# Performance work log

Measured on AMD Instinct MI355X. Metric: run time of the kernel, lower is better.

## Reference

```python
import jax, jax.numpy as jnp
import numpy as np

B, S, H, E, I_E, V = 4, 4096, 1024, 8, 512, 100000


def setup_inputs() -> dict:
    key = jax.random.key(0)
    k0, k1, k2, k3, k4, k5, k6 = jax.random.split(key, 7)
    hidden_states = jax.random.normal(k0, (B, S, H), dtype=jnp.float32)
    token_ids = jax.random.randint(k1, (B, S), 0, V, dtype=jnp.int64)
    mu = jax.random.normal(k2, (B, S, H), dtype=jnp.float32)
    # torch Linear(in,out,bias=False) weight is [out,in]; we store transposed [in,out]
    w_gate = jax.random.normal(k3, (E, H, I_E), dtype=jnp.float32) * 0.02
    w_up = jax.random.normal(k4, (E, H, I_E), dtype=jnp.float32) * 0.02
    w_down = jax.random.normal(k5, (E, I_E, H), dtype=jnp.float32) * 0.02
    # module zero-inits mu_router; use small random so the mu-override path is exercised
    mu_router_w = jax.random.normal(k6, (E, H), dtype=jnp.float32) * 0.02
    return {
        "hidden_states": hidden_states,
        "token_ids": token_ids,
        "mu": mu,
        "w_gate": w_gate,
        "w_up": w_up,
        "w_down": w_down,
        "mu_router_w": mu_router_w,
    }


def reference(hidden_states, token_ids, mu, w_gate, w_up, w_down, mu_router_w):
    num_experts = w_gate.shape[0]
    # deterministic token->expert mapping: token_id % num_experts (after clamp)
    tid = jnp.clip(token_ids, 0, V - 1)
    base_expert_ids = (tid % num_experts).astype(jnp.int32)  # [B,S]
    # mu-guided override: one_hot*10 + mu_logits, argmax
    mu_logits = jnp.einsum("bsh,eh->bse", mu, mu_router_w)
    base_one_hot = jax.nn.one_hot(base_expert_ids, num_experts, dtype=mu_logits.dtype)
    expert_ids = jnp.argmax(base_one_hot * 10.0 + mu_logits, axis=-1)  # [B,S]

    x = hidden_states.reshape(-1, H)          # [T,H], T=B*S
    eid = expert_ids.reshape(-1)              # [T]
    out = jnp.zeros_like(x)
    for e in range(num_experts):
        mask = (eid == e)[:, None]            # [T,1]
        g = x @ w_gate[e]                     # [T,I_E]
        u = x @ w_up[e]                       # [T,I_E]
        y = (jax.nn.silu(g) * u) @ w_down[e]  # [T,H] SwiGLU
        out = out + jnp.where(mask, y, 0.0)
    return out.reshape(hidden_states.shape)
```

## Files before the change

kernel.cpp:

```cpp
#include <hip/hip_runtime.h>
#include <stdint.h>

#define T_TOK   16384
#define H_DIM   1024
#define IE_DIM  512
#define E_NUM   8
#define V_MAX   100000

typedef __attribute__((ext_vector_type(8))) short bf16x8;
typedef __attribute__((ext_vector_type(4))) float f32x4;
typedef unsigned long long ull;

__device__ __forceinline__ unsigned short f2bf(float f) {
  union { float f; unsigned u; } v; v.f = f;
  unsigned r = v.u + 0x7fffu + ((v.u >> 16) & 1u);
  return (unsigned short)(r >> 16);
}

__device__ __forceinline__ void gload16(const void* g, void* l) {
  __builtin_amdgcn_global_load_lds(
      (const __attribute__((address_space(1))) unsigned int*)g,
      (__attribute__((address_space(3))) unsigned int*)(unsigned int)(uintptr_t)l,
      16, 0, 0);
}

__global__ __launch_bounds__(256) void k_pre(
    const float* __restrict__ mu, const int* __restrict__ tok,
    const float* __restrict__ mrw, int* __restrict__ eid,
    int* __restrict__ blockCnt,
    const float* __restrict__ wg, const float* __restrict__ wu,
    const float* __restrict__ wd, unsigned short* __restrict__ WgT,
    unsigned short* __restrict__ WuT, unsigned short* __restrict__ WdT) {
  __shared__ unsigned short lds[64][72];
  int tid = threadIdx.x;

  if (blockIdx.x < 1024) {
    int* cnt = (int*)&lds[0][0];
    if (tid < 8) cnt[tid] = 0;
    int wv = blockIdx.x * 4 + (tid >> 6);
    int t0 = wv * 4;
    int lane = tid & 63;
    const float4* mrw4 = (const float4*)mrw;

    float acc[4][E_NUM];
#pragma unroll
    for (int i = 0; i < 4; i++)
#pragma unroll
      for (int e = 0; e < E_NUM; e++) acc[i][e] = 0.f;

#pragma unroll
    for (int j = 0; j < 4; j++) {
      int idx = lane + 64 * j;
      float4 wr[E_NUM];
#pragma unroll
      for (int e = 0; e < E_NUM; e++) wr[e] = mrw4[e * 256 + idx];
#pragma unroll
      for (int i = 0; i < 4; i++) {
        float4 m = ((const float4*)(mu + (size_t)(t0 + i) * H_DIM))[idx];
#pragma unroll
        for (int e = 0; e < E_NUM; e++)
          acc[i][e] += m.x * wr[e].x + m.y * wr[e].y + m.z * wr[e].z + m.w * wr[e].w;
      }
    }
#pragma unroll
    for (int i = 0; i < 4; i++)
#pragma unroll
      for (int e = 0; e < E_NUM; e++)
#pragma unroll
        for (int off = 32; off >= 1; off >>= 1)
          acc[i][e] += __shfl_xor(acc[i][e], off, 64);

    __syncthreads();
#pragma unroll
    for (int i = 0; i < 4; i++) {
      int tv = tok[t0 + i];
      if (tv < 0) tv = 0;
      if (tv > V_MAX - 1) tv = V_MAX - 1;
      int base = tv & 7;
      int best = 0; float bs = -1e30f;
#pragma unroll
      for (int e = 0; e < E_NUM; e++) {
        float s = acc[i][e] + (e == base ? 10.f : 0.f);
        if (s > bs) { bs = s; best = e; }
      }
      if (lane == i) {
        eid[t0 + i] = best;
        atomicAdd(&cnt[best], 1);
      }
    }
    __syncthreads();
    if (tid < 8) blockCnt[blockIdx.x * 8 + tid] = cnt[tid];
  } else {
    int sel = (blockIdx.x - 1024) >> 10;
    int blk = blockIdx.x & 1023;
    const float* src; unsigned short* dst; int R, C;
    if (sel == 0)      { src = wg; dst = WgT; R = H_DIM; C = IE_DIM; }
    else if (sel == 1) { src = wu; dst = WuT; R = H_DIM; C = IE_DIM; }
    else               { src = wd; dst = WdT; R = IE_DIM; C = H_DIM; }
    int tpe = (R >> 6) * (C >> 6);
    int e = blk / tpe;
    int rem = blk % tpe;
    int tr = rem / (C >> 6);
    int tc = rem % (C >> 6);
    const float* s = src + (size_t)e * R * C;
    unsigned short* d = dst + (size_t)e * R * C;
    int r0 = tid >> 4;
    int c0 = (tid & 15) * 4;
#pragma unroll
    for (int i = 0; i < 4; i++) {
      int r = r0 + i * 16;
      float4 v = *(const float4*)(s + (size_t)(tr * 64 + r) * C + tc * 64 + c0);
      lds[r][c0 + 0] = f2bf(v.x); lds[r][c0 + 1] = f2bf(v.y);
      lds[r][c0 + 2] = f2bf(v.z); lds[r][c0 + 3] = f2bf(v.w);
    }
    __syncthreads();
    int oc = tid >> 2;
    int ob = (tid & 3) * 16;
    unsigned short tmp[16];
#pragma unroll
    for (int i = 0; i < 16; i++) tmp[i] = lds[ob + i][oc];
    uint4* dp = (uint4*)(d + (size_t)(tc * 64 + oc) * R + tr * 64 + ob);
    dp[0] = ((uint4*)tmp)[0];
    dp[1] = ((uint4*)tmp)[1];
  }
}

__global__ __launch_bounds__(1024) void k_scan2(
    const int* __restrict__ blockCnt, int* __restrict__ blockBase,
    int* __restrict__ offsets, int* __restrict__ tileOff,
    int* __restrict__ tileOff128) {
  int b = threadIdx.x;
  __shared__ ull s0[1024], s1[1024];
  __shared__ int offL[8];
  const int4* p = (const int4*)(blockCnt + b * 8);
  int4 x0 = p[0], x1 = p[1];
  int c[8] = {x0.x, x0.y, x0.z, x0.w, x1.x, x1.y, x1.z, x1.w};
  ull v0 = (ull)c[0] | ((ull)c[1] << 16) | ((ull)c[2] << 32) | ((ull)c[3] << 48);
  ull v1 = (ull)c[4] | ((ull)c[5] << 16) | ((ull)c[6] << 32) | ((ull)c[7] << 48);
  s0[b] = v0; s1[b] = v1;
  __syncthreads();
  for (int st = 1; st < 1024; st <<= 1) {
    ull a0 = 0, a1 = 0;
    if (b >= st) { a0 = s0[b - st]; a1 = s1[b - st]; }
    __syncthreads();
    v0 += a0; v1 += a1;
    s0[b] = v0; s1[b] = v1;
    __syncthreads();
  }
  if (b == 1023) {
    int tot[8];
#pragma unroll
    for (int e = 0; e < 4; e++) tot[e] = (int)((v0 >> (16 * e)) & 0xFFFF);
#pragma unroll
    for (int e = 0; e < 4; e++) tot[4 + e] = (int)((v1 >> (16 * e)) & 0xFFFF);
    int s = 0, ts = 0, ts2 = 0;
    for (int e = 0; e < E_NUM; e++) {
      offsets[e] = s; offL[e] = s;
      tileOff[e] = ts; tileOff128[e] = ts2;
      s += tot[e];
      ts += (tot[e] + 255) >> 8;
      ts2 += (tot[e] + 127) >> 7;
    }
    offsets[E_NUM] = s; tileOff[E_NUM] = ts; tileOff128[E_NUM] = ts2;
  }
  __syncthreads();
  int be[8];
#pragma unroll
  for (int e = 0; e < 4; e++)
    be[e] = offL[e] + (int)((v0 >> (16 * e)) & 0xFFFF) - c[e];
#pragma unroll
  for (int e = 0; e < 4; e++)
    be[4 + e] = offL[4 + e] + (int)((v1 >> (16 * e)) & 0xFFFF) - c[4 + e];
  int4* q = (int4*)(blockBase + b * 8);
  q[0] = make_int4(be[0], be[1], be[2], be[3]);
  q[1] = make_int4(be[4], be[5], be[6], be[7]);
}

__global__ __launch_bounds__(256) void k_gather(
    const float* __restrict__ hs, const int* __restrict__ eid,
    const int* __restrict__ blockBase, int* __restrict__ tokofrow,
    unsigned short* __restrict__ Xs) {
  int b = blockIdx.x;
  int tid = threadIdx.x;
  __shared__ int eL[16];
  __shared__ int posL[16];
  if (tid < 16) eL[tid] = eid[b * 16 + tid];
  __syncthreads();
  if (tid < 16) {
    int e = eL[tid];
    int r = 0;
    for (int j = 0; j < tid; j++) r += (eL[j] == e);
    int pos = blockBase[b * 8 + e] + r;
    posL[tid] = pos;
    tokofrow[pos] = b * 16 + tid;
  }
  __syncthreads();
  int w = tid >> 6, lane = tid & 63;
#pragma unroll
  for (int i = 0; i < 4; i++) {
    int li = w * 4 + i;
    int t = b * 16 + li;
    int pos = posL[li];
    const float4* src = (const float4*)(hs + (size_t)t * H_DIM);
    unsigned short* drow = Xs + (size_t)pos * H_DIM;
#pragma unroll
    for (int j = 0; j < 4; j++) {
      float4 v = src[lane + 64 * j];
      ushort4 bb;
      bb.x = f2bf(v.x); bb.y = f2bf(v.y); bb.z = f2bf(v.z); bb.w = f2bf(v.w);
      *(ushort4*)(drow + (lane + 64 * j) * 4) = bb;
    }
  }
}

__global__ __launch_bounds__(512, 1) void k_gemm1(
    const unsigned short* __restrict__ Xs,
    const unsigned short* __restrict__ WgT,
    const unsigned short* __restrict__ WuT,
    unsigned short* __restrict__ Hb,
    const int* __restrict__ offsets, const int* __restrict__ tileOff) {
  int bid0 = blockIdx.x;
  int xcd = bid0 & 7, seq = bid0 >> 3;
  int wg = (xcd < 4 ? xcd * 36 : 144 + (xcd - 4) * 35) + seq;
  int nt = wg & 3;
  int mlin = wg >> 2;
  if (mlin >= tileOff[E_NUM]) return;
  int e = 0;
#pragma unroll
  for (int i = 1; i < E_NUM; i++)
    if (mlin >= tileOff[i]) e = i;
  int mtile = mlin - tileOff[e];
  int segStart = offsets[e], segEnd = offsets[e + 1];
  int M = segEnd - segStart;

  __shared__ unsigned short Alds[2][256 * 64];
  __shared__ unsigned short Bglds[2][128 * 64];
  __shared__ unsigned short Bulds[2][128 * 64];

  int tid = threadIdx.x;
  int lane = tid & 63;
  int w = tid >> 6;
  int wm = w >> 1;
  int wn = w & 1;
  int r0 = lane & 15;
  int kcb = lane >> 4;

  f32x4 accg[4][4], accu[4][4];
#pragma unroll
  for (int i = 0; i < 4; i++)
#pragma unroll
    for (int j = 0; j < 4; j++) {
      accg[i][j] = (f32x4)(0.f);
      accu[i][j] = (f32x4)(0.f);
    }

  const unsigned short* Asrc[4];
#pragma unroll
  for (int i = 0; i < 4; i++) {
    int s = tid + i * 512;
    int row = s >> 3;
    int ch = (s & 7) ^ (row & 7);
    int gr = mtile * 256 + row; if (gr > M - 1) gr = M - 1;
    Asrc[i] = Xs + (size_t)(segStart + gr) * H_DIM + ch * 8;
  }
  const unsigned short* Bgsrc[2];
  const unsigned short* Busrc[2];
#pragma unroll
  for (int i = 0; i < 2; i++) {
    int s = tid + i * 512;
    int row = s >> 3;
    int ch = (s & 7) ^ (row & 7);
    Bgsrc[i] = WgT + (size_t)e * IE_DIM * H_DIM + (size_t)(nt * 128 + row) * H_DIM + ch * 8;
    Busrc[i] = WuT + (size_t)e * IE_DIM * H_DIM + (size_t)(nt * 128 + row) * H_DIM + ch * 8;
  }

#define GLA(i, kt, buf) gload16(Asrc[i] + (kt) * 64, (char*)Alds[buf] + (tid + (i) * 512) * 16)
#define GLG(i, kt, buf) gload16(Bgsrc[i] + (kt) * 64, (char*)Bglds[buf] + (tid + (i) * 512) * 16)
#define GLU(i, kt, buf) gload16(Busrc[i] + (kt) * 64, (char*)Bulds[buf] + (tid + (i) * 512) * 16)

  int aoff[4][2], boff[4][2];
#pragma unroll
  for (int mf = 0; mf < 4; mf++) {
    int row = wm * 64 + mf * 16 + r0;
#pragma unroll
    for (int ks = 0; ks < 2; ks++) {
      int c = ks * 4 + kcb;
      aoff[mf][ks] = row * 128 + ((c ^ (row & 7)) << 4);
    }
  }
#pragma unroll
  for (int nf = 0; nf < 4; nf++) {
    int row = wn * 64 + nf * 16 + r0;
#pragma unroll
    for (int ks = 0; ks < 2; ks++) {
      int c = ks * 4 + kcb;
      boff[nf][ks] = row * 128 + ((c ^ (row & 7)) << 4);
    }
  }

  const int NT = H_DIM / 64;
  GLA(0, 0, 0); GLA(1, 0, 0); GLA(2, 0, 0); GLA(3, 0, 0);
  GLG(0, 0, 0); GLG(1, 0, 0); GLU(0, 0, 0); GLU(1, 0, 0);

  bf16x8 a0[2][2], a1[2][2], bb[4][2];

  for (int kt = 0; kt < NT; kt++) {
    int buf = kt & 1, nbuf = buf ^ 1;
    int ktn = (kt + 1 < NT) ? kt + 1 : 0;
    const char* Ab = (const char*)Alds[buf];
    const char* Bgb = (const char*)Bglds[buf];
    const char* Bub = (const char*)Bulds[buf];

    __builtin_amdgcn_s_barrier();
    GLA(0, ktn, nbuf); GLA(1, ktn, nbuf); GLA(2, ktn, nbuf); GLA(3, ktn, nbuf);
    GLG(0, ktn, nbuf); GLG(1, ktn, nbuf); GLU(0, ktn, nbuf); GLU(1, ktn, nbuf);
    asm volatile("s_waitcnt vmcnt(8)" ::: "memory");
    __builtin_amdgcn_s_barrier();

#pragma unroll
    for (int mf = 0; mf < 2; mf++)
#pragma unroll
      for (int ks = 0; ks < 2; ks++)
        a0[mf][ks] = *(const bf16x8*)(Ab + aoff[mf][ks]);
#pragma unroll
    for (int nf = 0; nf < 4; nf++)
#pragma unroll
      for (int ks = 0; ks < 2; ks++)
        bb[nf][ks] = *(const bf16x8*)(Bgb + boff[nf][ks]);
    asm volatile("s_waitcnt lgkmcnt(0)" ::: "memory");
    __builtin_amdgcn_sched_barrier(0);
    __builtin_amdgcn_s_setprio(1);
#pragma unroll
    for (int mf = 0; mf < 2; mf++)
#pragma unroll
      for (int nf = 0; nf < 4; nf++)
#pragma unroll
        for (int ks = 0; ks < 2; ks++)
          accg[mf][nf] = __builtin_amdgcn_mfma_f32_16x16x32_bf16(
              a0[mf][ks], bb[nf][ks], accg[mf][nf], 0, 0, 0);
    __builtin_amdgcn_s_setprio(0);

#pragma unroll
    for (int mf = 0; mf < 2; mf++)
#pragma unroll
      for (int ks = 0; ks < 2; ks++)
        a1[mf][ks] = *(const bf16x8*)(Ab + aoff[2 + mf][ks]);
    asm volatile("s_waitcnt lgkmcnt(0)" ::: "memory");
    __builtin_amdgcn_sched_barrier(0);
    __builtin_amdgcn_s_setprio(1);
#pragma unroll
    for (int mf = 0; mf < 2; mf++)
#pragma unroll
      for (int nf = 0; nf < 4; nf++)
#pragma unroll
        for (int ks = 0; ks < 2; ks++)
          accg[2 + mf][nf] = __builtin_amdgcn_mfma_f32_16x16x32_bf16(
              a1[mf][ks], bb[nf][ks], accg[2 + mf][nf], 0, 0, 0);
    __builtin_amdgcn_s_setprio(0);

#pragma unroll
    for (int nf = 0; nf < 4; nf++)
#pragma unroll
      for (int ks = 0; ks < 2; ks++)
        bb[nf][ks] = *(const bf16x8*)(Bub + boff[nf][ks]);
    asm volatile("s_waitcnt lgkmcnt(0)" ::: "memory");
    __builtin_amdgcn_sched_barrier(0);
    __builtin_amdgcn_s_setprio(1);
#pragma unroll
    for (int mf = 0; mf < 2; mf++)
#pragma unroll
      for (int nf = 0; nf < 4; nf++)
#pragma unroll
        for (int ks = 0; ks < 2; ks++)
          accu[mf][nf] = __builtin_amdgcn_mfma_f32_16x16x32_bf16(
              a0[mf][ks], bb[nf][ks], accu[mf][nf], 0, 0, 0);
    __builtin_amdgcn_s_setprio(0);

    __builtin_amdgcn_s_setprio(1);
#pragma unroll
    for (int mf = 0; mf < 2; mf++)
#pragma unroll
      for (int nf = 0; nf < 4; nf++)
#pragma unroll
        for (int ks = 0; ks < 2; ks++)
          accu[2 + mf][nf] = __builtin_amdgcn_mfma_f32_16x16x32_bf16(
              a1[mf][ks], bb[nf][ks], accu[2 + mf][nf], 0, 0, 0);
    __builtin_amdgcn_s_setprio(0);
  }
  asm volatile("s_waitcnt vmcnt(0)" ::: "memory");
#undef GLA
#undef GLG
#undef GLU

  int rowBase = segStart + mtile * 256 + wm * 64;
#pragma unroll
  for (int mf = 0; mf < 4; mf++)
#pragma unroll
    for (int nf = 0; nf < 4; nf++) {
      int col = nt * 128 + wn * 64 + nf * 16 + r0;
#pragma unroll
      for (int j = 0; j < 4; j++) {
        int r = rowBase + mf * 16 + (lane >> 4) * 4 + j;
        if (r < segEnd) {
          float g = accg[mf][nf][j];
          float u = accu[mf][nf][j];
          float h = (g / (1.f + __expf(-g))) * u;
          Hb[(size_t)r * IE_DIM + col] = f2bf(h);
        }
      }
    }
}

__global__ __launch_bounds__(512) void k_gemm2(
    const unsigned short* __restrict__ Hb,
    const unsigned short* __restrict__ WdT,
    float* __restrict__ out,
    const int* __restrict__ offsets, const int* __restrict__ tileOff,
    const int* __restrict__ tokofrow) {
  int bid0 = blockIdx.x;
  int wg = (bid0 & 7) * 135 + (bid0 >> 3);
  int nt = wg & 7;
  int mlin = wg >> 3;
  if (mlin >= tileOff[E_NUM]) return;
  int e = 0;
#pragma unroll
  for (int i = 1; i < E_NUM; i++)
    if (mlin >= tileOff[i]) e = i;
  int mtile = mlin - tileOff[e];
  int segStart = offsets[e], segEnd = offsets[e + 1];
  int M = segEnd - segStart;

  __shared__ unsigned short Alds[3][128 * 32];
  __shared__ unsigned short Blds[3][128 * 32];

  int tid = threadIdx.x;
  int lane = tid & 63;
  int w = tid >> 6;
  int wm = w >> 2;
  int wn = w & 3;

  f32x4 acc[4][2];
#pragma unroll
  for (int i = 0; i < 4; i++)
#pragma unroll
    for (int j = 0; j < 2; j++) acc[i][j] = (f32x4)(0.f);

  int sr = tid >> 2;
  int sc = tid & 3;
  int scc = sc ^ ((sr >> 1) & 3);
  int grow = mtile * 128 + sr;
  if (grow > M - 1) grow = M - 1;
  const unsigned short* Arow = Hb + (size_t)(segStart + grow) * IE_DIM + scc * 8;
  const unsigned short* Brow =
      WdT + (size_t)e * H_DIM * IE_DIM + (size_t)(nt * 128 + sr) * IE_DIM + scc * 8;

#define STAGE2(buf, k0)                                            \
  {                                                                \
    gload16(Arow + (k0), (char*)Alds[buf] + tid * 16);             \
    gload16(Brow + (k0), (char*)Blds[buf] + tid * 16);             \
  }

  int kc = lane >> 4;
  int arow[4], browv[2];
#pragma unroll
  for (int mf = 0; mf < 4; mf++) arow[mf] = wm * 64 + mf * 16 + (lane & 15);
#pragma unroll
  for (int nf = 0; nf < 2; nf++) browv[nf] = wn * 32 + nf * 16 + (lane & 15);

  const int NT = IE_DIM / 32;
  STAGE2(0, 0);
  STAGE2(1, 32);

  int cur = 0;
  for (int t = 0; t < NT; t++) {
    asm volatile("s_waitcnt vmcnt(2)" ::: "memory");
    __builtin_amdgcn_s_barrier();
    __builtin_amdgcn_sched_barrier(0);
    int tn = t + 2; if (tn >= NT) tn -= NT;
    int nbuf = cur + 2; if (nbuf >= 3) nbuf -= 3;
    STAGE2(nbuf, tn * 32);

    bf16x8 a[4], b[2];
#pragma unroll
    for (int mf = 0; mf < 4; mf++) {
      int row = arow[mf];
      int byte = row * 64 + ((kc ^ ((row >> 1) & 3)) << 4);
      a[mf] = *(const bf16x8*)((const char*)Alds[cur] + byte);
    }
#pragma unroll
    for (int nf = 0; nf < 2; nf++) {
      int row = browv[nf];
      int byte = row * 64 + ((kc ^ ((row >> 1) & 3)) << 4);
      b[nf] = *(const bf16x8*)((const char*)Blds[cur] + byte);
    }
    __builtin_amdgcn_s_setprio(1);
#pragma unroll
    for (int mf = 0; mf < 4; mf++)
#pragma unroll
      for (int nf = 0; nf < 2; nf++)
        acc[mf][nf] = __builtin_amdgcn_mfma_f32_16x16x32_bf16(
            a[mf], b[nf], acc[mf][nf], 0, 0, 0);
    __builtin_amdgcn_s_setprio(0);
    cur = (cur + 1 == 3) ? 0 : cur + 1;
  }
#undef STAGE2
  asm volatile("s_waitcnt vmcnt(0)" ::: "memory");

  int rowBase = segStart + mtile * 128 + wm * 64;
#pragma unroll
  for (int mf = 0; mf < 4; mf++)
#pragma unroll
    for (int nf = 0; nf < 2; nf++) {
      int col = nt * 128 + wn * 32 + nf * 16 + (lane & 15);
#pragma unroll
      for (int j = 0; j < 4; j++) {
        int r = rowBase + mf * 16 + (lane >> 4) * 4 + j;
        if (r < segEnd) {
          int t = tokofrow[r];
          out[(size_t)t * H_DIM + col] = acc[mf][nf][j];
        }
      }
    }
}

#define WS_XS    ((size_t)0)
#define WS_WGT   ((size_t)33554432)
#define WS_WUT   ((size_t)41943040)
#define WS_WDT   ((size_t)50331648)
#define WS_HB    ((size_t)58720256)
#define WS_EID   ((size_t)75497472)
#define WS_TOK   ((size_t)75563008)
#define WS_OFF   ((size_t)75628544)
#define WS_BC    ((size_t)75629568)
#define WS_BB    ((size_t)75662336)

extern "C" void kernel_launch(void* const* d_in, const int* in_sizes, int n_in,
                              void* d_out, int out_size, void* d_ws, size_t ws_size,
                              hipStream_t stream) {
  const float* hs  = (const float*)d_in[0];
  const int*   tok = (const int*)d_in[1];
  const float* mu  = (const float*)d_in[2];
  const float* wg  = (const float*)d_in[3];
  const float* wu  = (const float*)d_in[4];
  const float* wd  = (const float*)d_in[5];
  const float* mrw = (const float*)d_in[6];
  float* out = (float*)d_out;
  char* ws = (char*)d_ws;

  unsigned short* Xs  = (unsigned short*)(ws + WS_XS);
  unsigned short* WgT = (unsigned short*)(ws + WS_WGT);
  unsigned short* WuT = (unsigned short*)(ws + WS_WUT);
  unsigned short* WdT = (unsigned short*)(ws + WS_WDT);
  unsigned short* Hb  = (unsigned short*)(ws + WS_HB);
  int* eid      = (int*)(ws + WS_EID);
  int* tokofrow = (int*)(ws + WS_TOK);
  int* offsets   = (int*)(ws + WS_OFF);
  int* tileOff   = offsets + 16;
  int* tileOff128= offsets + 32;
  int* blockCnt = (int*)(ws + WS_BC);
  int* blockBase= (int*)(ws + WS_BB);

  k_pre<<<4096, 256, 0, stream>>>(mu, tok, mrw, eid, blockCnt,
                                  wg, wu, wd, WgT, WuT, WdT);
  k_scan2<<<1, 1024, 0, stream>>>(blockCnt, blockBase, offsets, tileOff, tileOff128);
  k_gather<<<1024, 256, 0, stream>>>(hs, eid, blockBase, tokofrow, Xs);
  k_gemm1<<<284, 512, 0, stream>>>(Xs, WgT, WuT, Hb, offsets, tileOff);
  k_gemm2<<<135 * 8, 512, 0, stream>>>(Hb, WdT, out, offsets, tileOff128, tokofrow);
}
```

Before: 169.0 us.

## Deepen gate/up GEMM pipeline to 4-stage K=32 buffers with interleaved loads

Rewrites the gate/up grouped GEMM main loop. It moves from a double-buffered K=64 tile to a quad-buffered K=32 ring, with prefetch three stages ahead. Global-to-LDS loads are split into four pieces (A halves, gate, up) and placed between MFMA phases, with a new 4-way XOR swizzle. The goal is deeper latency hiding and finer overlap of memory and compute. In exchange the loop has many more s_barriers per K step and the MFMA work per phase is smaller.

```diff
diff --git a/kernel.cpp b/kernel.cpp
--- a/kernel.cpp
+++ b/kernel.cpp
@@ -233,9 +233,9 @@
   int segStart = offsets[e], segEnd = offsets[e + 1];
   int M = segEnd - segStart;
 
-  __shared__ unsigned short Alds[2][256 * 64];
-  __shared__ unsigned short Bglds[2][128 * 64];
-  __shared__ unsigned short Bulds[2][128 * 64];
+  __shared__ unsigned short Alds[4][256 * 32];
+  __shared__ unsigned short Bglds[4][128 * 32];
+  __shared__ unsigned short Bulds[4][128 * 32];
 
   int tid = threadIdx.x;
   int lane = tid & 63;
@@ -254,143 +254,123 @@
       accu[i][j] = (f32x4)(0.f);
     }
 
-  const unsigned short* Asrc[4];
-#pragma unroll
-  for (int i = 0; i < 4; i++) {
-    int s = tid + i * 512;
-    int row = s >> 3;
-    int ch = (s & 7) ^ (row & 7);
-    int gr = mtile * 256 + row; if (gr > M - 1) gr = M - 1;
-    Asrc[i] = Xs + (size_t)(segStart + gr) * H_DIM + ch * 8;
-  }
-  const unsigned short* Bgsrc[2];
-  const unsigned short* Busrc[2];
-#pragma unroll
-  for (int i = 0; i < 2; i++) {
-    int s = tid + i * 512;
-    int row = s >> 3;
-    int ch = (s & 7) ^ (row & 7);
-    Bgsrc[i] = WgT + (size_t)e * IE_DIM * H_DIM + (size_t)(nt * 128 + row) * H_DIM + ch * 8;
-    Busrc[i] = WuT + (size_t)e * IE_DIM * H_DIM + (size_t)(nt * 128 + row) * H_DIM + ch * 8;
-  }
-
-#define GLA(i, kt, buf) gload16(Asrc[i] + (kt) * 64, (char*)Alds[buf] + (tid + (i) * 512) * 16)
-#define GLG(i, kt, buf) gload16(Bgsrc[i] + (kt) * 64, (char*)Bglds[buf] + (tid + (i) * 512) * 16)
-#define GLU(i, kt, buf) gload16(Busrc[i] + (kt) * 64, (char*)Bulds[buf] + (tid + (i) * 512) * 16)
-
-  int aoff[4][2], boff[4][2];
+  int arow0 = tid >> 2;
+  int arow1 = arow0 + 128;
+  int acs = (tid & 3) ^ ((arow0 >> 1) & 3);
+  int ga0 = mtile * 256 + arow0; if (ga0 > M - 1) ga0 = M - 1;
+  int ga1 = mtile * 256 + arow1; if (ga1 > M - 1) ga1 = M - 1;
+  const unsigned short* Aad0 = Xs + (size_t)(segStart + ga0) * H_DIM + acs * 8;
+  const unsigned short* Aad1 = Xs + (size_t)(segStart + ga1) * H_DIM + acs * 8;
+  int brow = tid >> 2;
+  int bcs = (tid & 3) ^ ((brow >> 1) & 3);
+  const unsigned short* Bgad =
+      WgT + (size_t)e * IE_DIM * H_DIM + (size_t)(nt * 128 + brow) * H_DIM + bcs * 8;
+  const unsigned short* Buad =
+      WuT + (size_t)e * IE_DIM * H_DIM + (size_t)(nt * 128 + brow) * H_DIM + bcs * 8;
+
+#define SGA0(h) gload16(Aad0 + ((h) & 31) * 32, (char*)Alds + ((h) & 3) * 16384 + tid * 16)
+#define SGA1(h) gload16(Aad1 + ((h) & 31) * 32, (char*)Alds + ((h) & 3) * 16384 + 8192 + tid * 16)
+#define SGG(h)  gload16(Bgad + ((h) & 31) * 32, (char*)Bglds + ((h) & 3) * 8192 + tid * 16)
+#define SGU(h)  gload16(Buad + ((h) & 31) * 32, (char*)Bulds + ((h) & 3) * 8192 + tid * 16)
+
+  int aoff[4], boff[4];
 #pragma unroll
   for (int mf = 0; mf < 4; mf++) {
     int row = wm * 64 + mf * 16 + r0;
-#pragma unroll
-    for (int ks = 0; ks < 2; ks++) {
-      int c = ks * 4 + kcb;
-      aoff[mf][ks] = row * 128 + ((c ^ (row & 7)) << 4);
-    }
+    aoff[mf] = row * 64 + ((kcb ^ ((row >> 1) & 3)) << 4);
   }
 #pragma unroll
   for (int nf = 0; nf < 4; nf++) {
     int row = wn * 64 + nf * 16 + r0;
-#pragma unroll
-    for (int ks = 0; ks < 2; ks++) {
-      int c = ks * 4 + kcb;
-      boff[nf][ks] = row * 128 + ((c ^ (row & 7)) << 4);
-    }
-  }
-
-  const int NT = H_DIM / 64;
-  GLA(0, 0, 0); GLA(1, 0, 0); GLA(2, 0, 0); GLA(3, 0, 0);
-  GLG(0, 0, 0); GLG(1, 0, 0); GLU(0, 0, 0); GLU(1, 0, 0);
-
-  bf16x8 a0[2][2], a1[2][2], bb[4][2];
-
-  for (int kt = 0; kt < NT; kt++) {
-    int buf = kt & 1, nbuf = buf ^ 1;
-    int ktn = (kt + 1 < NT) ? kt + 1 : 0;
-    const char* Ab = (const char*)Alds[buf];
-    const char* Bgb = (const char*)Bglds[buf];
-    const char* Bub = (const char*)Bulds[buf];
-
-    __builtin_amdgcn_s_barrier();
-    GLA(0, ktn, nbuf); GLA(1, ktn, nbuf); GLA(2, ktn, nbuf); GLA(3, ktn, nbuf);
-    GLG(0, ktn, nbuf); GLG(1, ktn, nbuf); GLU(0, ktn, nbuf); GLU(1, ktn, nbuf);
-    asm volatile("s_waitcnt vmcnt(8)" ::: "memory");
-    __builtin_amdgcn_s_barrier();
-
-#pragma unroll
-    for (int mf = 0; mf < 2; mf++)
-#pragma unroll
-      for (int ks = 0; ks < 2; ks++)
-        a0[mf][ks] = *(const bf16x8*)(Ab + aoff[mf][ks]);
-#pragma unroll
-    for (int nf = 0; nf < 4; nf++)
-#pragma unroll
-      for (int ks = 0; ks < 2; ks++)
-        bb[nf][ks] = *(const bf16x8*)(Bgb + boff[nf][ks]);
-    asm volatile("s_waitcnt lgkmcnt(0)" ::: "memory");
-    __builtin_amdgcn_sched_barrier(0);
-    __builtin_amdgcn_s_setprio(1);
-#pragma unroll
-    for (int mf = 0; mf < 2; mf++)
-#pragma unroll
-      for (int nf = 0; nf < 4; nf++)
-#pragma unroll
-        for (int ks = 0; ks < 2; ks++)
+    boff[nf] = row * 64 + ((kcb ^ ((row >> 1) & 3)) << 4);
+  }
+
+  SGA0(0); SGA1(0); SGG(0); SGU(0);
+  SGA0(1); SGA1(1); SGG(1); SGU(1);
+  SGA0(2); SGA1(2); SGG(2); SGU(2);
+  asm volatile("s_waitcnt vmcnt(8)" ::: "memory");
+  __builtin_amdgcn_s_barrier();
+
+  const int NH = H_DIM / 32;
+  for (int hh = 0; hh < NH; hh += 4) {
+#pragma unroll
+    for (int u = 0; u < 4; u++) {
+      int h = hh + u;
+      const char* Ab  = (const char*)Alds + u * 16384;
+      const char* Bgb = (const char*)Bglds + u * 8192;
+      const char* Bub = (const char*)Bulds + u * 8192;
+      int hn = h + 3;
+      bf16x8 a[4], bg[4], bu[4];
+
+      a[0] = *(const bf16x8*)(Ab + aoff[0]);
+      a[1] = *(const bf16x8*)(Ab + aoff[1]);
+#pragma unroll
+      for (int nf = 0; nf < 4; nf++) bg[nf] = *(const bf16x8*)(Bgb + boff[nf]);
+      SGA0(hn);
+      __builtin_amdgcn_s_barrier();
+      asm volatile("s_waitcnt lgkmcnt(0)" ::: "memory");
+      __builtin_amdgcn_sched_barrier(0);
+      __builtin_amdgcn_s_setprio(1);
+#pragma unroll
+      for (int mf = 0; mf < 2; mf++)
+#pragma unroll
+        for (int nf = 0; nf < 4; nf++)
           accg[mf][nf] = __builtin_amdgcn_mfma_f32_16x16x32_bf16(
-              a0[mf][ks], bb[nf][ks], accg[mf][nf], 0, 0, 0);
-    __builtin_amdgcn_s_setprio(0);
-
-#pragma unroll
-    for (int mf = 0; mf < 2; mf++)
-#pragma unroll
-      for (int ks = 0; ks < 2; ks++)
-        a1[mf][ks] = *(const bf16x8*)(Ab + aoff[2 + mf][ks]);
-    asm volatile("s_waitcnt lgkmcnt(0)" ::: "memory");
-    __builtin_amdgcn_sched_barrier(0);
-    __builtin_amdgcn_s_setprio(1);
-#pragma unroll
-    for (int mf = 0; mf < 2; mf++)
-#pragma unroll
-      for (int nf = 0; nf < 4; nf++)
-#pragma unroll
-        for (int ks = 0; ks < 2; ks++)
+              a[mf], bg[nf], accg[mf][nf], 0, 0, 0);
+      __builtin_amdgcn_s_setprio(0);
+      __builtin_amdgcn_s_barrier();
+
+      a[2] = *(const bf16x8*)(Ab + aoff[2]);
+      a[3] = *(const bf16x8*)(Ab + aoff[3]);
+      SGA1(hn);
+      __builtin_amdgcn_s_barrier();
+      asm volatile("s_waitcnt lgkmcnt(0)" ::: "memory");
+      __builtin_amdgcn_sched_barrier(0);
+      __builtin_amdgcn_s_setprio(1);
+#pragma unroll
+      for (int mf = 0; mf < 2; mf++)
+#pragma unroll
+        for (int nf = 0; nf < 4; nf++)
           accg[2 + mf][nf] = __builtin_amdgcn_mfma_f32_16x16x32_bf16(
-              a1[mf][ks], bb[nf][ks], accg[2 + mf][nf], 0, 0, 0);
-    __builtin_amdgcn_s_setprio(0);
-
-#pragma unroll
-    for (int nf = 0; nf < 4; nf++)
-#pragma unroll
-      for (int ks = 0; ks < 2; ks++)
-        bb[nf][ks] = *(const bf16x8*)(Bub + boff[nf][ks]);
-    asm volatile("s_waitcnt lgkmcnt(0)" ::: "memory");
-    __builtin_amdgcn_sched_barrier(0);
-    __builtin_amdgcn_s_setprio(1);
-#pragma unroll
-    for (int mf = 0; mf < 2; mf++)
-#pragma unroll
-      for (int nf = 0; nf < 4; nf++)
-#pragma unroll
-        for (int ks = 0; ks < 2; ks++)
+              a[2 + mf], bg[nf], accg[2 + mf][nf], 0, 0, 0);
+      __builtin_amdgcn_s_setprio(0);
+      __builtin_amdgcn_s_barrier();
+
+#pragma unroll
+      for (int nf = 0; nf < 4; nf++) bu[nf] = *(const bf16x8*)(Bub + boff[nf]);
+      SGG(hn);
+      __builtin_amdgcn_s_barrier();
+      asm volatile("s_waitcnt lgkmcnt(0)" ::: "memory");
+      __builtin_amdgcn_sched_barrier(0);
+      __builtin_amdgcn_s_setprio(1);
+#pragma unroll
+      for (int mf = 0; mf < 2; mf++)
+#pragma unroll
+        for (int nf = 0; nf < 4; nf++)
           accu[mf][nf] = __builtin_amdgcn_mfma_f32_16x16x32_bf16(
-              a0[mf][ks], bb[nf][ks], accu[mf][nf], 0, 0, 0);
-    __builtin_amdgcn_s_setprio(0);
-
-    __builtin_amdgcn_s_setprio(1);
-#pragma unroll
-    for (int mf = 0; mf < 2; mf++)
-#pragma unroll
-      for (int nf = 0; nf < 4; nf++)
-#pragma unroll
-        for (int ks = 0; ks < 2; ks++)
+              a[mf], bu[nf], accu[mf][nf], 0, 0, 0);
+      __builtin_amdgcn_s_setprio(0);
+      __builtin_amdgcn_s_barrier();
+
+      SGU(hn);
+      asm volatile("s_waitcnt vmcnt(8)" ::: "memory");
+      __builtin_amdgcn_s_barrier();
+      __builtin_amdgcn_s_setprio(1);
+#pragma unroll
+      for (int mf = 0; mf < 2; mf++)
+#pragma unroll
+        for (int nf = 0; nf < 4; nf++)
           accu[2 + mf][nf] = __builtin_amdgcn_mfma_f32_16x16x32_bf16(
-              a1[mf][ks], bb[nf][ks], accu[2 + mf][nf], 0, 0, 0);
-    __builtin_amdgcn_s_setprio(0);
+              a[2 + mf], bu[nf], accu[2 + mf][nf], 0, 0, 0);
+      __builtin_amdgcn_s_setprio(0);
+      __builtin_amdgcn_s_barrier();
+    }
   }
   asm volatile("s_waitcnt vmcnt(0)" ::: "memory");
-#undef GLA
-#undef GLG
-#undef GLU
+#undef SGA0
+#undef SGA1
+#undef SGG
+#undef SGU
 
   int rowBase = segStart + mtile * 256 + wm * 64;
 #pragma unroll
```

Measured after the change: 167.0 us. About the same (-1.2%).
